# Performance work log

Measured on AMD Instinct MI355X. Metric: run time of the kernel, lower is better.

The kernel has to match this reference:

```python
import jax, jax.numpy as jnp
import numpy as np

EPS = 1e-5
HD = 16          # hidden_dim
OC = 256         # out_chs
NH = 8           # num_heads (groups of qkv conv)
DV = OC // (2 * HD)  # per-head value dim = 8


def conv_bn_silu(x, w, gamma, beta, mean, var, stride=1, pad=1, groups=1):
    # Conv2d(bias=False) + BatchNorm2d(eval) + SiLU, NCHW/OIHW
    y = jax.lax.conv_general_dilated(
        x, w, (stride, stride), [(pad, pad), (pad, pad)],
        dimension_numbers=('NCHW', 'OIHW', 'NCHW'),
        feature_group_count=groups)
    inv = gamma * jax.lax.rsqrt(var + EPS)
    y = y * inv[None, :, None, None] + (beta - mean * inv)[None, :, None, None]
    return y * jax.nn.sigmoid(y)


def _bn_params(key, c):
    k1, k2, k3, k4 = jax.random.split(key, 4)
    g = 1.0 + 0.1 * jax.random.normal(k1, (c,), jnp.float32)
    b = 0.1 * jax.random.normal(k2, (c,), jnp.float32)
    m = 0.1 * jax.random.normal(k3, (c,), jnp.float32)
    v = jax.random.uniform(k4, (c,), jnp.float32, 0.5, 1.5)
    return g, b, m, v


def setup_inputs() -> dict:
    key = jax.random.key(0)
    ks = jax.random.split(key, 8)
    B, C, H, W = 16, 256, 80, 80
    qkv_out = HD * 2 + OC // 2  # 160
    d = {}
    d['x'] = jax.random.normal(ks[0], (B, C, H, W), jnp.float32)
    # qkv_conv: grouped 3x3, groups=NH -> in per group = C//NH
    d['qkv_w'] = jax.random.normal(ks[1], (qkv_out, C // NH, 3, 3), jnp.float32) * 0.05
    d['qkv_g'], d['qkv_b'], d['qkv_m'], d['qkv_v'] = _bn_params(ks[2], qkv_out)
    # hidden_conv: dense 3x3
    d['hid_w'] = jax.random.normal(ks[3], (OC, C, 3, 3), jnp.float32) * 0.02
    d['hid_g'], d['hid_b'], d['hid_m'], d['hid_v'] = _bn_params(ks[4], OC)
    # out_conv: 1x1 on (OC//2*3) channels
    d['out_w'] = jax.random.normal(ks[5], (OC, OC // 2 * 3, 1, 1), jnp.float32) * 0.05
    d['out_g'], d['out_b'], d['out_m'], d['out_v'] = _bn_params(ks[6], OC)
    return d


def reference(x, qkv_w, qkv_g, qkv_b, qkv_m, qkv_v,
              hid_w, hid_g, hid_b, hid_m, hid_v,
              out_w, out_g, out_b, out_m, out_v):
    B, C, H, W = x.shape
    N = H * W
    qkv = conv_bn_silu(x, qkv_w, qkv_g, qkv_b, qkv_m, qkv_v, stride=1, pad=1, groups=NH)
    q = qkv[:, :HD]               # (B, HD, H, W)
    k = qkv[:, HD:2 * HD]
    v = qkv[:, 2 * HD:]           # (B, OC//2, H, W)
    # permute to (B, N, HD) / (B, N, HD, DV), channel-major reshape matches torch .view
    q = q.transpose(0, 2, 3, 1).reshape(B, N, HD)
    k = k.transpose(0, 2, 3, 1).reshape(B, N, HD)
    v = v.transpose(0, 2, 3, 1).reshape(B, N, HD, DV)
    # per-pixel tiny attention: attn[b,n,i,j] = softmax_j(q_i * k_j)
    attn = jax.nn.softmax(q[..., :, None] * k[..., None, :], axis=-1)  # (B,N,HD,HD)
    y = jnp.einsum('bnij,bnjd->bnid', attn, v)                          # (B,N,HD,DV)
    # torch: permute(0,2,3,1).view(B, OC//2, H, W)
    y = y.transpose(0, 2, 3, 1).reshape(B, OC // 2, H, W)
    h = conv_bn_silu(x, hid_w, hid_g, hid_b, hid_m, hid_v, stride=1, pad=1)
    y = jnp.concatenate([y, h], axis=1)  # (B, OC//2*3, H, W)
    return conv_bn_silu(y, out_w, out_g, out_b, out_m, out_v, stride=1, pad=0)
```

## Files before the change

kernel.cpp:

```cpp
#include <hip/hip_runtime.h>
#include <stdint.h>

typedef unsigned short u16;
typedef unsigned int u32;
typedef __attribute__((ext_vector_type(4))) float f32x4;
typedef __attribute__((ext_vector_type(8))) __bf16 bf16x8;

#define EPS_BN 1e-5f

__device__ __forceinline__ u16 f2bf(float f) {
  u32 u = __builtin_bit_cast(u32, f);
  u32 r = (u + 0x7fffu + ((u >> 16) & 1u)) >> 16;
  return (u16)r;
}

__device__ __forceinline__ float silu_f(float v) {
  return v / (1.0f + __expf(-v));
}

__device__ __forceinline__ void gll16(const void* g, void* l) {
  __builtin_amdgcn_global_load_lds(
      (__attribute__((address_space(1))) void*)(void*)g,
      (__attribute__((address_space(3))) void*)l, 16, 0, 0);
}

__global__ __launch_bounds__(256) void prep(
    const float* __restrict__ qkv_w, const float* __restrict__ qg,
    const float* __restrict__ qb, const float* __restrict__ qm,
    const float* __restrict__ qv,
    const float* __restrict__ hid_w, const float* __restrict__ hg,
    const float* __restrict__ hb, const float* __restrict__ hm,
    const float* __restrict__ hv,
    const float* __restrict__ out_w, const float* __restrict__ og,
    const float* __restrict__ ob, const float* __restrict__ om,
    const float* __restrict__ ov,
    u16* __restrict__ wtb, u16* __restrict__ w2b, u16* __restrict__ wqp,
    float* __restrict__ bnq_s, float* __restrict__ bnq_b,
    float* __restrict__ bnh_s, float* __restrict__ bnh_b,
    float* __restrict__ bn2s, float* __restrict__ bn2b,
    float* __restrict__ zpg)
{
  const int gid = blockIdx.x * 256 + threadIdx.x;
  if (gid < 256 * 2304) {
    int j = gid / 2304, k = gid - j * 2304;
    int tap = k >> 8, c = k & 255;
    wtb[gid] = f2bf(hid_w[(j * 256 + c) * 9 + tap]);
  }
  if (gid < 73728) {
    int g = gid / 9216;
    int r = gid - g * 9216;
    int j = r / 288, k = r - j * 288;
    int tap = k >> 5, cg = k & 31;
    float v = 0.f;
    if (j < 20) v = qkv_w[((g * 20 + j) * 32 + cg) * 9 + tap];
    wqp[gid] = f2bf(v);
  }
  if (gid < 98304) w2b[gid] = f2bf(out_w[gid]);
  if (gid < 160) {
    float iv = qg[gid] * rsqrtf(qv[gid] + EPS_BN);
    bnq_s[gid] = iv; bnq_b[gid] = qb[gid] - qm[gid] * iv;
  }
  if (gid < 256) {
    float iv = hg[gid] * rsqrtf(hv[gid] + EPS_BN);
    bnh_s[gid] = iv; bnh_b[gid] = hb[gid] - hm[gid] * iv;
    float iv2 = og[gid] * rsqrtf(ov[gid] + EPS_BN);
    bn2s[gid] = iv2; bn2b[gid] = ob[gid] - om[gid] * iv2;
  }
  if (gid < 64) zpg[gid] = 0.f;
}

__global__ __launch_bounds__(256) void nchw2nhwc(
    const float* __restrict__ x, u16* __restrict__ xn)
{
  __shared__ u16 T[80 * 66];
  const int t = threadIdx.x;
  const int ct = blockIdx.x;
  const int h  = blockIdx.y;
  const int b  = blockIdx.z;
  const float* src = x + ((size_t)b * 256 + ct * 64) * 6400 + h * 80;
  for (int it = 0; it < 20; ++it) {
    int idx = it * 256 + t;
    int cl = idx / 80, wl = idx - cl * 80;
    T[wl * 66 + cl] = f2bf(src[(size_t)cl * 6400 + wl]);
  }
  __syncthreads();
  u16* dst = xn + ((size_t)(b * 80 + h) * 80) * 256 + ct * 64;
  for (int it = 0; it < 5; ++it) {
    int idx = it * 256 + t;
    int wl = idx >> 4;
    int cl = (idx & 15) * 4;
    ushort4 v4;
    v4.x = T[wl * 66 + cl + 0];
    v4.y = T[wl * 66 + cl + 1];
    v4.z = T[wl * 66 + cl + 2];
    v4.w = T[wl * 66 + cl + 3];
    *(ushort4*)(dst + (size_t)wl * 256 + cl) = v4;
  }
}

__global__ __launch_bounds__(256, 2) void gemm_main(
    const u16* __restrict__ xn, const u16* __restrict__ wt,
    const float* __restrict__ bns, const float* __restrict__ bnb,
    const float* __restrict__ zpg, u16* __restrict__ ycat)
{
  __shared__ __attribute__((aligned(16))) u16 Al[128 * 64];
  __shared__ __attribute__((aligned(16))) u16 Bl[128 * 64];
  const int t = threadIdx.x;
  const int wave = t >> 6, lane = t & 63;
  const int wr = wave >> 1, wc = wave & 1;
  const int orig = blockIdx.y * 2 + blockIdx.x;
  const int wg = (orig & 7) * 200 + (orig >> 3);
  const int jtile = (wg / 800) * 128;
  const int ptile = (wg % 800) * 128;

  const int srcc = (((lane & 7) ^ ((lane >> 3) & 7)) * 8);
  int pb[4], hh[4], wwv[4], bofB[4];
#pragma unroll
  for (int c = 0; c < 4; ++c) {
    int m = wave * 32 + c * 8 + (lane >> 3);
    int p = ptile + m;
    pb[c] = p;
    int hw = p % 6400;
    hh[c] = hw / 80;
    wwv[c] = hw - (hw / 80) * 80;
    bofB[c] = (jtile + m) * 2304 + srcc;
  }
  u16* AlW = Al + wave * 2048;
  u16* BlW = Bl + wave * 2048;

  f32x4 acc[4][4];
#pragma unroll
  for (int m = 0; m < 4; ++m)
#pragma unroll
    for (int n = 0; n < 4; ++n) {
      f32x4 z = {0.f, 0.f, 0.f, 0.f};
      acc[m][n] = z;
    }

  for (int ks = 0; ks < 36; ++ks) {
    const int k0 = ks * 64;
    const int tap = k0 >> 8;
    const int c0 = k0 & 255;
    const int dh = tap / 3 - 1, dw = tap - (tap / 3) * 3 - 1;
    __syncthreads();
#pragma unroll
    for (int c = 0; c < 4; ++c) {
      int h2 = hh[c] + dh, w2 = wwv[c] + dw;
      bool ok = ((unsigned)h2 < 80u) & ((unsigned)w2 < 80u);
      const u16* src = ok
          ? (xn + ((size_t)(pb[c] + dh * 80 + dw) * 256 + c0 + srcc))
          : (const u16*)zpg;
      gll16(src, AlW + c * 512);
    }
#pragma unroll
    for (int c = 0; c < 4; ++c)
      gll16(wt + (size_t)(bofB[c] + k0), BlW + c * 512);
    __syncthreads();
#pragma unroll
    for (int kk = 0; kk < 2; ++kk) {
      const int q = kk * 4 + (lane >> 4);
      const int c16 = lane & 15;
      bf16x8 av[4], bv[4];
#pragma unroll
      for (int m = 0; m < 4; ++m) {
        int r = wr * 64 + m * 16 + c16;
        av[m] = *(const bf16x8*)(Al + r * 64 + (q ^ (r & 7)) * 8);
      }
#pragma unroll
      for (int n = 0; n < 4; ++n) {
        int r = wc * 64 + n * 16 + c16;
        bv[n] = *(const bf16x8*)(Bl + r * 64 + (q ^ (r & 7)) * 8);
      }
#pragma unroll
      for (int m = 0; m < 4; ++m)
#pragma unroll
        for (int n = 0; n < 4; ++n)
          acc[m][n] = __builtin_amdgcn_mfma_f32_16x16x32_bf16(
              av[m], bv[n], acc[m][n], 0, 0, 0);
    }
  }

  const int c16 = lane & 15, rg = lane >> 4;
#pragma unroll
  for (int n = 0; n < 4; ++n) {
    int j = jtile + wc * 64 + n * 16 + c16;
    float sc = bns[j], bi = bnb[j];
#pragma unroll
    for (int m = 0; m < 4; ++m) {
      int p0 = ptile + wr * 64 + m * 16 + rg * 4;
#pragma unroll
      for (int r = 0; r < 4; ++r) {
        float v = silu_f(acc[m][n][r] * sc + bi);
        ycat[(size_t)(p0 + r) * 384 + 128 + j] = f2bf(v);
      }
    }
  }
}

__global__ __launch_bounds__(256) void qkv_gemm(
    const u16* __restrict__ xn, const u16* __restrict__ wqp,
    const float* __restrict__ bnq_s, const float* __restrict__ bnq_b,
    float* __restrict__ qkvb)
{
  __shared__ __attribute__((aligned(16))) u16 Bs[32 * 296];
  const int t = threadIdx.x;
  const int wave = t >> 6, lane = t & 63;
  const int g = blockIdx.y;
  const int pt0 = blockIdx.x * 256;

  for (int idx = t; idx < 9216; idx += 256) {
    int j = idx / 288, k = idx - j * 288;
    Bs[j * 296 + k] = wqp[(size_t)(g * 32 + j) * 288 + k];
  }
  __syncthreads();

  const int c16 = lane & 15, q = lane >> 4;
  int pix[4], ph[4], pw[4];
#pragma unroll
  for (int m = 0; m < 4; ++m) {
    pix[m] = pt0 + wave * 64 + m * 16 + c16;
    int hw = pix[m] % 6400;
    ph[m] = hw / 80;
    pw[m] = hw - (hw / 80) * 80;
  }
  f32x4 acc[4][2];
#pragma unroll
  for (int m = 0; m < 4; ++m)
#pragma unroll
    for (int n = 0; n < 2; ++n) {
      f32x4 z = {0.f, 0.f, 0.f, 0.f};
      acc[m][n] = z;
    }
  bf16x8 zv;
#pragma unroll
  for (int i = 0; i < 8; ++i) zv[i] = (__bf16)0.0f;

#pragma unroll
  for (int tap = 0; tap < 9; ++tap) {
    const int dh = tap / 3 - 1, dw = tap - (tap / 3) * 3 - 1;
    const int dp = dh * 80 + dw;
    const bf16x8 bv0 = *(const bf16x8*)(Bs + c16 * 296 + tap * 32 + q * 8);
    const bf16x8 bv1 = *(const bf16x8*)(Bs + (16 + c16) * 296 + tap * 32 + q * 8);
#pragma unroll
    for (int m = 0; m < 4; ++m) {
      bool ok = ((unsigned)(ph[m] + dh) < 80u) & ((unsigned)(pw[m] + dw) < 80u);
      const bf16x8 raw = *(const bf16x8*)(
          xn + (long)(pix[m] + dp) * 256 + g * 32 + q * 8);
      const bf16x8 av = ok ? raw : zv;
      acc[m][0] = __builtin_amdgcn_mfma_f32_16x16x32_bf16(av, bv0, acc[m][0], 0, 0, 0);
      acc[m][1] = __builtin_amdgcn_mfma_f32_16x16x32_bf16(av, bv1, acc[m][1], 0, 0, 0);
    }
  }

#pragma unroll
  for (int n = 0; n < 2; ++n) {
    int jj = n * 16 + c16;
    if (jj < 20) {
      int oc = g * 20 + jj;
      float sc = bnq_s[oc], bi = bnq_b[oc];
#pragma unroll
      for (int m = 0; m < 4; ++m) {
        int p0 = pt0 + wave * 64 + m * 16 + q * 4;
#pragma unroll
        for (int r = 0; r < 4; ++r)
          qkvb[(size_t)(p0 + r) * 160 + oc] = silu_f(acc[m][n][r] * sc + bi);
      }
    }
  }
}

__global__ __launch_bounds__(256) void attn_k(
    const float* __restrict__ qkvb, u16* __restrict__ ycat)
{
  __shared__ float qs[16 * 168];
  const int t = threadIdx.x;
  const size_t p0 = (size_t)blockIdx.x * 16;
  const float* src = qkvb + p0 * 160;
  for (int idx = t; idx < 2560; idx += 256) {
    int r = idx / 160;
    qs[r * 168 + (idx - r * 160)] = src[idx];
  }
  __syncthreads();
  const int px = t >> 4, i = t & 15;
  const float* row = qs + px * 168;
  const float qi = row[i];
  float s[16];
  float mx = -3.4e38f;
#pragma unroll
  for (int j = 0; j < 16; ++j) { s[j] = qi * row[16 + j]; mx = fmaxf(mx, s[j]); }
  float sum = 0.f;
#pragma unroll
  for (int j = 0; j < 16; ++j) { s[j] = __expf(s[j] - mx); sum += s[j]; }
  const float inv = 1.0f / sum;
  float y[8];
#pragma unroll
  for (int d = 0; d < 8; ++d) y[d] = 0.f;
#pragma unroll
  for (int j = 0; j < 16; ++j) {
    const float a = s[j];
    const float* vr = row + 32 + j * 8;
#pragma unroll
    for (int d = 0; d < 8; ++d) y[d] += a * vr[d];
  }
  union { u16 u[8]; uint4 v4; } pk;
#pragma unroll
  for (int d = 0; d < 8; ++d) pk.u[d] = f2bf(y[d] * inv);
  *(uint4*)(ycat + (p0 + px) * 384 + i * 8) = pk.v4;
}

__global__ __launch_bounds__(256, 2) void gemm_out(
    const u16* __restrict__ w2, const u16* __restrict__ ycat,
    const float* __restrict__ bns, const float* __restrict__ bnb,
    float* __restrict__ out)
{
  __shared__ __attribute__((aligned(16))) u16 Al[128 * 64];
  __shared__ __attribute__((aligned(16))) u16 Bl[128 * 64];
  const int t = threadIdx.x;
  const int wave = t >> 6, lane = t & 63;
  const int wr = wave >> 1, wc = wave & 1;
  const int orig = blockIdx.y * 2 + blockIdx.x;
  const int wg = (orig & 7) * 200 + (orig >> 3);
  const int octile = (wg / 800) * 128;
  const int ptile = (wg % 800) * 128;

  const int srcc = (((lane & 7) ^ ((lane >> 3) & 7)) * 8);
  int bofA[4], bofB[4];
#pragma unroll
  for (int c = 0; c < 4; ++c) {
    int m = wave * 32 + c * 8 + (lane >> 3);
    bofA[c] = (octile + m) * 384 + srcc;
    bofB[c] = (ptile + m) * 384 + srcc;
  }
  u16* AlW = Al + wave * 2048;
  u16* BlW = Bl + wave * 2048;

  f32x4 acc[4][4];
#pragma unroll
  for (int m = 0; m < 4; ++m)
#pragma unroll
    for (int n = 0; n < 4; ++n) {
      f32x4 z = {0.f, 0.f, 0.f, 0.f};
      acc[m][n] = z;
    }

  for (int ks = 0; ks < 6; ++ks) {
    const int k0 = ks * 64;
    __syncthreads();
#pragma unroll
    for (int c = 0; c < 4; ++c) gll16(w2 + (size_t)(bofA[c] + k0), AlW + c * 512);
#pragma unroll
    for (int c = 0; c < 4; ++c) gll16(ycat + (size_t)(bofB[c] + k0), BlW + c * 512);
    __syncthreads();
#pragma unroll
    for (int kk = 0; kk < 2; ++kk) {
      const int q = kk * 4 + (lane >> 4);
      const int c16 = lane & 15;
      bf16x8 av[4], bv[4];
#pragma unroll
      for (int m = 0; m < 4; ++m) {
        int r = wr * 64 + m * 16 + c16;
        av[m] = *(const bf16x8*)(Al + r * 64 + (q ^ (r & 7)) * 8);
      }
#pragma unroll
      for (int n = 0; n < 4; ++n) {
        int r = wc * 64 + n * 16 + c16;
        bv[n] = *(const bf16x8*)(Bl + r * 64 + (q ^ (r & 7)) * 8);
      }
#pragma unroll
      for (int m = 0; m < 4; ++m)
#pragma unroll
        for (int n = 0; n < 4; ++n)
          acc[m][n] = __builtin_amdgcn_mfma_f32_16x16x32_bf16(
              av[m], bv[n], acc[m][n], 0, 0, 0);
    }
  }

  const int c16 = lane & 15, rg = lane >> 4;
  const int b = ptile / 6400;
  const int hwb = ptile - b * 6400;
#pragma unroll
  for (int m = 0; m < 4; ++m) {
    int oc0 = octile + wr * 64 + m * 16 + rg * 4;
#pragma unroll
    for (int n = 0; n < 4; ++n) {
      int hw = hwb + wc * 64 + n * 16 + c16;
#pragma unroll
      for (int r = 0; r < 4; ++r) {
        int oc = oc0 + r;
        float v = silu_f(acc[m][n][r] * bns[oc] + bnb[oc]);
        out[((size_t)b * 256 + oc) * 6400 + hw] = v;
      }
    }
  }
}

extern "C" void kernel_launch(void* const* d_in, const int* in_sizes, int n_in,
                              void* d_out, int out_size, void* d_ws, size_t ws_size,
                              hipStream_t stream) {
  (void)in_sizes; (void)n_in; (void)out_size; (void)ws_size;
  const float* x    = (const float*)d_in[0];
  const float* qkvw = (const float*)d_in[1];
  const float* qg   = (const float*)d_in[2];
  const float* qb   = (const float*)d_in[3];
  const float* qm   = (const float*)d_in[4];
  const float* qv   = (const float*)d_in[5];
  const float* hw_  = (const float*)d_in[6];
  const float* hg   = (const float*)d_in[7];
  const float* hb   = (const float*)d_in[8];
  const float* hm   = (const float*)d_in[9];
  const float* hv   = (const float*)d_in[10];
  const float* ow   = (const float*)d_in[11];
  const float* og   = (const float*)d_in[12];
  const float* ob   = (const float*)d_in[13];
  const float* om   = (const float*)d_in[14];
  const float* ov   = (const float*)d_in[15];

  char* ws = (char*)d_ws;
  float* zpg   = (float*)(ws + 0);
  float* bnq_s = (float*)(ws + 256);
  float* bnq_b = (float*)(ws + 1280);
  float* bnh_s = (float*)(ws + 2304);
  float* bnh_b = (float*)(ws + 3328);
  float* bn2s  = (float*)(ws + 4352);
  float* bn2b  = (float*)(ws + 5376);
  u16*   wtb   = (u16*)(ws + 6400);
  u16*   w2b   = (u16*)(ws + 1186048);
  u16*   wqp   = (u16*)(ws + 1382656);
  u16*   xn    = (u16*)(ws + 1536000);
  float* qkvb  = (float*)(ws + 53964800);
  u16*   ycat  = (u16*)(ws + 119500800);
  float* out   = (float*)d_out;

  prep<<<dim3(2304), dim3(256), 0, stream>>>(
      qkvw, qg, qb, qm, qv, hw_, hg, hb, hm, hv, ow, og, ob, om, ov,
      wtb, w2b, wqp, bnq_s, bnq_b, bnh_s, bnh_b, bn2s, bn2b, zpg);
  nchw2nhwc<<<dim3(4, 80, 16), dim3(256), 0, stream>>>(x, xn);
  gemm_main<<<dim3(2, 800), dim3(256), 0, stream>>>(
      xn, wtb, bnh_s, bnh_b, zpg, ycat);
  qkv_gemm<<<dim3(400, 8), dim3(256), 0, stream>>>(
      xn, wqp, bnq_s, bnq_b, qkvb);
  attn_k<<<dim3(6400), dim3(256), 0, stream>>>(qkvb, ycat);
  gemm_out<<<dim3(2, 800), dim3(256), 0, stream>>>(
      w2b, ycat, bn2s, bn2b, out);
}
```

Measured before the change: 356.0 us.

## Restructure grouped qkv conv to stage all-group pixel tiles via LDS async loads

The grouped 3x3 qkv convolution now runs one block per 128-pixel tile across all 8 groups. Each 64-channel input slice is staged into swizzled LDS with global_load_lds and padding is redirected to a zero buffer. This replaces the old per-group grid, where each block re-read strided 16-byte chunks straight from global memory. Separately, the NCHW-to-NHWC transpose now reads float4 vectors instead of scalars. The new qkv kernel holds 32 accumulator fragments per thread, which raises register pressure, and it loads weights from global memory on every k-step.

```diff
diff --git a/kernel.cpp b/kernel.cpp
--- a/kernel.cpp
+++ b/kernel.cpp
@@ -78,10 +78,14 @@
   const int h  = blockIdx.y;
   const int b  = blockIdx.z;
   const float* src = x + ((size_t)b * 256 + ct * 64) * 6400 + h * 80;
-  for (int it = 0; it < 20; ++it) {
+  for (int it = 0; it < 5; ++it) {
     int idx = it * 256 + t;
-    int cl = idx / 80, wl = idx - cl * 80;
-    T[wl * 66 + cl] = f2bf(src[(size_t)cl * 6400 + wl]);
+    int cl = idx / 20, w4 = idx - cl * 20;
+    float4 v = *(const float4*)(src + (size_t)cl * 6400 + w4 * 4);
+    T[(w4 * 4 + 0) * 66 + cl] = f2bf(v.x);
+    T[(w4 * 4 + 1) * 66 + cl] = f2bf(v.y);
+    T[(w4 * 4 + 2) * 66 + cl] = f2bf(v.z);
+    T[(w4 * 4 + 3) * 66 + cl] = f2bf(v.w);
   }
   __syncthreads();
   u16* dst = xn + ((size_t)(b * 80 + h) * 80) * 256 + ct * 64;
@@ -197,74 +201,98 @@
   }
 }
 
-__global__ __launch_bounds__(256) void qkv_gemm(
+__global__ __launch_bounds__(256, 2) void qkv_gemm(
     const u16* __restrict__ xn, const u16* __restrict__ wqp,
     const float* __restrict__ bnq_s, const float* __restrict__ bnq_b,
-    float* __restrict__ qkvb)
-{
-  __shared__ __attribute__((aligned(16))) u16 Bs[32 * 296];
+    const float* __restrict__ zpg, float* __restrict__ qkvb)
+{
+  __shared__ __attribute__((aligned(16))) u16 Al[128 * 64];
   const int t = threadIdx.x;
   const int wave = t >> 6, lane = t & 63;
-  const int g = blockIdx.y;
-  const int pt0 = blockIdx.x * 256;
-
-  for (int idx = t; idx < 9216; idx += 256) {
-    int j = idx / 288, k = idx - j * 288;
-    Bs[j * 296 + k] = wqp[(size_t)(g * 32 + j) * 288 + k];
-  }
-  __syncthreads();
-
-  const int c16 = lane & 15, q = lane >> 4;
-  int pix[4], ph[4], pw[4];
-#pragma unroll
-  for (int m = 0; m < 4; ++m) {
-    pix[m] = pt0 + wave * 64 + m * 16 + c16;
-    int hw = pix[m] % 6400;
-    ph[m] = hw / 80;
-    pw[m] = hw - (hw / 80) * 80;
-  }
-  f32x4 acc[4][2];
-#pragma unroll
-  for (int m = 0; m < 4; ++m)
-#pragma unroll
-    for (int n = 0; n < 2; ++n) {
+  const int orig = blockIdx.x;
+  const int wg = (orig & 7) * 100 + (orig >> 3);
+  const int ptile = wg * 128;
+
+  const int srcc = (((lane & 7) ^ ((lane >> 3) & 7)) * 8);
+  int pb[4], hh[4], wwv[4];
+#pragma unroll
+  for (int c = 0; c < 4; ++c) {
+    int m = wave * 32 + c * 8 + (lane >> 3);
+    int p = ptile + m;
+    pb[c] = p;
+    int hw = p % 6400;
+    hh[c] = hw / 80;
+    wwv[c] = hw - (hw / 80) * 80;
+  }
+  u16* AlW = Al + wave * 2048;
+
+  const int q = lane >> 4, c16 = lane & 15;
+  f32x4 acc[2][16];
+#pragma unroll
+  for (int m = 0; m < 2; ++m)
+#pragma unroll
+    for (int f = 0; f < 16; ++f) {
       f32x4 z = {0.f, 0.f, 0.f, 0.f};
-      acc[m][n] = z;
-    }
-  bf16x8 zv;
-#pragma unroll
-  for (int i = 0; i < 8; ++i) zv[i] = (__bf16)0.0f;
-
-#pragma unroll
-  for (int tap = 0; tap < 9; ++tap) {
+      acc[m][f] = z;
+    }
+
+  for (int ks = 0; ks < 36; ++ks) {
+    const int k0 = ks * 64;
+    const int tap = k0 >> 8;
+    const int c0 = k0 & 255;
+    const int cc = ks & 3;
     const int dh = tap / 3 - 1, dw = tap - (tap / 3) * 3 - 1;
-    const int dp = dh * 80 + dw;
-    const bf16x8 bv0 = *(const bf16x8*)(Bs + c16 * 296 + tap * 32 + q * 8);
-    const bf16x8 bv1 = *(const bf16x8*)(Bs + (16 + c16) * 296 + tap * 32 + q * 8);
-#pragma unroll
-    for (int m = 0; m < 4; ++m) {
-      bool ok = ((unsigned)(ph[m] + dh) < 80u) & ((unsigned)(pw[m] + dw) < 80u);
-      const bf16x8 raw = *(const bf16x8*)(
-          xn + (long)(pix[m] + dp) * 256 + g * 32 + q * 8);
-      const bf16x8 av = ok ? raw : zv;
-      acc[m][0] = __builtin_amdgcn_mfma_f32_16x16x32_bf16(av, bv0, acc[m][0], 0, 0, 0);
-      acc[m][1] = __builtin_amdgcn_mfma_f32_16x16x32_bf16(av, bv1, acc[m][1], 0, 0, 0);
-    }
-  }
-
-#pragma unroll
-  for (int n = 0; n < 2; ++n) {
-    int jj = n * 16 + c16;
-    if (jj < 20) {
-      int oc = g * 20 + jj;
-      float sc = bnq_s[oc], bi = bnq_b[oc];
-#pragma unroll
-      for (int m = 0; m < 4; ++m) {
-        int p0 = pt0 + wave * 64 + m * 16 + q * 4;
-#pragma unroll
-        for (int r = 0; r < 4; ++r)
-          qkvb[(size_t)(p0 + r) * 160 + oc] = silu_f(acc[m][n][r] * sc + bi);
-      }
+    __syncthreads();
+#pragma unroll
+    for (int c = 0; c < 4; ++c) {
+      int h2 = hh[c] + dh, w2 = wwv[c] + dw;
+      bool ok = ((unsigned)h2 < 80u) & ((unsigned)w2 < 80u);
+      const u16* src = ok
+          ? (xn + ((size_t)(pb[c] + dh * 80 + dw) * 256 + c0 + srcc))
+          : (const u16*)zpg;
+      gll16(src, AlW + c * 512);
+    }
+    bf16x8 bv[2][2];
+#pragma unroll
+    for (int h = 0; h < 2; ++h)
+#pragma unroll
+      for (int nf = 0; nf < 2; ++nf) {
+        int row = (2 * cc + h) * 32 + nf * 16 + c16;
+        bv[h][nf] = *(const bf16x8*)(wqp + (size_t)row * 288 + tap * 32 + q * 8);
+      }
+    __syncthreads();
+    bf16x8 av[2][2];
+#pragma unroll
+    for (int m = 0; m < 2; ++m) {
+      int r = wave * 32 + m * 16 + c16;
+#pragma unroll
+      for (int h = 0; h < 2; ++h) {
+        int q8 = h * 4 + q;
+        av[m][h] = *(const bf16x8*)(Al + r * 64 + (q8 ^ (r & 7)) * 8);
+      }
+    }
+#pragma unroll
+    for (int h = 0; h < 2; ++h)
+#pragma unroll
+      for (int m = 0; m < 2; ++m)
+#pragma unroll
+        for (int nf = 0; nf < 2; ++nf)
+          acc[m][(2 * cc + h) * 2 + nf] = __builtin_amdgcn_mfma_f32_16x16x32_bf16(
+              av[m][h], bv[h][nf], acc[m][(2 * cc + h) * 2 + nf], 0, 0, 0);
+  }
+
+#pragma unroll
+  for (int f = 0; f < 16; ++f) {
+    int jj = (f & 1) * 16 + c16;
+    if (jj >= 20) continue;
+    int oc = (f >> 1) * 20 + jj;
+    float sc = bnq_s[oc], bi = bnq_b[oc];
+#pragma unroll
+    for (int m = 0; m < 2; ++m) {
+      int p0 = ptile + wave * 32 + m * 16 + q * 4;
+#pragma unroll
+      for (int r = 0; r < 4; ++r)
+        qkvb[(size_t)(p0 + r) * 160 + oc] = silu_f(acc[m][f][r] * sc + bi);
     }
   }
 }
@@ -437,8 +465,8 @@
   nchw2nhwc<<<dim3(4, 80, 16), dim3(256), 0, stream>>>(x, xn);
   gemm_main<<<dim3(2, 800), dim3(256), 0, stream>>>(
       xn, wtb, bnh_s, bnh_b, zpg, ycat);
-  qkv_gemm<<<dim3(400, 8), dim3(256), 0, stream>>>(
-      xn, wqp, bnq_s, bnq_b, qkvb);
+  qkv_gemm<<<dim3(800), dim3(256), 0, stream>>>(
+      xn, wqp, bnq_s, bnq_b, zpg, qkvb);
   attn_k<<<dim3(6400), dim3(256), 0, stream>>>(qkvb, ycat);
   gemm_out<<<dim3(2, 800), dim3(256), 0, stream>>>(
       w2b, ycat, bn2s, bn2b, out);
```

After: 749.7 us. 2.11x slower.

## Fuse grouped qkv conv into main hidden-conv GEMM and vectorize NCHW transpose loads

Applied to the files above, without the earlier changes.

Drops the separate qkv_gemm kernel. The grouped 3x3 qkv convolution is now computed inside gemm_main, reusing the activation tiles already staged in LDS. Each output-column tile handles the qkv groups whose 32 input channels fall in its k-slice, and the weights come straight from global memory. This removes a second full read of xn and one kernel launch, at the cost of 64 extra accumulator registers per thread, which may hurt occupancy under launch_bounds(256,2). The NCHW-to-NHWC transpose also switches to float4 global loads.

```diff
diff --git a/kernel.cpp b/kernel.cpp
--- a/kernel.cpp
+++ b/kernel.cpp
@@ -78,10 +78,14 @@
   const int h  = blockIdx.y;
   const int b  = blockIdx.z;
   const float* src = x + ((size_t)b * 256 + ct * 64) * 6400 + h * 80;
-  for (int it = 0; it < 20; ++it) {
+  for (int it = 0; it < 5; ++it) {
     int idx = it * 256 + t;
-    int cl = idx / 80, wl = idx - cl * 80;
-    T[wl * 66 + cl] = f2bf(src[(size_t)cl * 6400 + wl]);
+    int cl = idx / 20, w4 = idx - cl * 20;
+    float4 v = *(const float4*)(src + (size_t)cl * 6400 + w4 * 4);
+    T[(w4 * 4 + 0) * 66 + cl] = f2bf(v.x);
+    T[(w4 * 4 + 1) * 66 + cl] = f2bf(v.y);
+    T[(w4 * 4 + 2) * 66 + cl] = f2bf(v.z);
+    T[(w4 * 4 + 3) * 66 + cl] = f2bf(v.w);
   }
   __syncthreads();
   u16* dst = xn + ((size_t)(b * 80 + h) * 80) * 256 + ct * 64;
@@ -100,8 +104,11 @@
 
 __global__ __launch_bounds__(256, 2) void gemm_main(
     const u16* __restrict__ xn, const u16* __restrict__ wt,
+    const u16* __restrict__ wqp,
     const float* __restrict__ bns, const float* __restrict__ bnb,
-    const float* __restrict__ zpg, u16* __restrict__ ycat)
+    const float* __restrict__ bnq_s, const float* __restrict__ bnq_b,
+    const float* __restrict__ zpg, u16* __restrict__ ycat,
+    float* __restrict__ qkvb)
 {
   __shared__ __attribute__((aligned(16))) u16 Al[128 * 64];
   __shared__ __attribute__((aligned(16))) u16 Bl[128 * 64];
@@ -110,7 +117,8 @@
   const int wr = wave >> 1, wc = wave & 1;
   const int orig = blockIdx.y * 2 + blockIdx.x;
   const int wg = (orig & 7) * 200 + (orig >> 3);
-  const int jtile = (wg / 800) * 128;
+  const int jt = wg / 800;
+  const int jtile = jt * 128;
   const int ptile = (wg % 800) * 128;
 
   const int srcc = (((lane & 7) ^ ((lane >> 3) & 7)) * 8);
@@ -128,6 +136,8 @@
   u16* AlW = Al + wave * 2048;
   u16* BlW = Bl + wave * 2048;
 
+  const int c16 = lane & 15, lq = lane >> 4;
+
   f32x4 acc[4][4];
 #pragma unroll
   for (int m = 0; m < 4; ++m)
@@ -136,51 +146,81 @@
       f32x4 z = {0.f, 0.f, 0.f, 0.f};
       acc[m][n] = z;
     }
-
-  for (int ks = 0; ks < 36; ++ks) {
-    const int k0 = ks * 64;
-    const int tap = k0 >> 8;
-    const int c0 = k0 & 255;
+  f32x4 acc_q[2][8];
+#pragma unroll
+  for (int m = 0; m < 2; ++m)
+#pragma unroll
+    for (int f = 0; f < 8; ++f) {
+      f32x4 z = {0.f, 0.f, 0.f, 0.f};
+      acc_q[m][f] = z;
+    }
+
+  for (int tap = 0; tap < 9; ++tap) {
     const int dh = tap / 3 - 1, dw = tap - (tap / 3) * 3 - 1;
-    __syncthreads();
+    const int dp = dh * 80 + dw;
+    const u16* srcA[4];
 #pragma unroll
     for (int c = 0; c < 4; ++c) {
       int h2 = hh[c] + dh, w2 = wwv[c] + dw;
       bool ok = ((unsigned)h2 < 80u) & ((unsigned)w2 < 80u);
-      const u16* src = ok
-          ? (xn + ((size_t)(pb[c] + dh * 80 + dw) * 256 + c0 + srcc))
-          : (const u16*)zpg;
-      gll16(src, AlW + c * 512);
-    }
-#pragma unroll
-    for (int c = 0; c < 4; ++c)
-      gll16(wt + (size_t)(bofB[c] + k0), BlW + c * 512);
-    __syncthreads();
-#pragma unroll
-    for (int kk = 0; kk < 2; ++kk) {
-      const int q = kk * 4 + (lane >> 4);
-      const int c16 = lane & 15;
-      bf16x8 av[4], bv[4];
-#pragma unroll
-      for (int m = 0; m < 4; ++m) {
-        int r = wr * 64 + m * 16 + c16;
-        av[m] = *(const bf16x8*)(Al + r * 64 + (q ^ (r & 7)) * 8);
-      }
-#pragma unroll
-      for (int n = 0; n < 4; ++n) {
-        int r = wc * 64 + n * 16 + c16;
-        bv[n] = *(const bf16x8*)(Bl + r * 64 + (q ^ (r & 7)) * 8);
-      }
-#pragma unroll
-      for (int m = 0; m < 4; ++m)
-#pragma unroll
-        for (int n = 0; n < 4; ++n)
-          acc[m][n] = __builtin_amdgcn_mfma_f32_16x16x32_bf16(
-              av[m], bv[n], acc[m][n], 0, 0, 0);
-    }
-  }
-
-  const int c16 = lane & 15, rg = lane >> 4;
+      srcA[c] = ok ? (xn + ((size_t)(pb[c] + dp) * 256 + srcc))
+                   : (const u16*)zpg;
+    }
+#pragma unroll
+    for (int cc = 0; cc < 4; ++cc) {
+      const int c0 = cc * 64;
+      const int k0 = tap * 256 + c0;
+      __syncthreads();
+#pragma unroll
+      for (int c = 0; c < 4; ++c)
+        gll16(srcA[c] == (const u16*)zpg ? srcA[c] : srcA[c] + c0,
+              AlW + c * 512);
+#pragma unroll
+      for (int c = 0; c < 4; ++c)
+        gll16(wt + (size_t)(bofB[c] + k0), BlW + c * 512);
+      const int gq = 2 * cc + jt;
+      const bf16x8 bq0 = *(const bf16x8*)(
+          wqp + ((size_t)(gq * 32) + c16) * 288 + tap * 32 + lq * 8);
+      const bf16x8 bq1 = *(const bf16x8*)(
+          wqp + ((size_t)(gq * 32) + 16 + c16) * 288 + tap * 32 + lq * 8);
+      __syncthreads();
+#pragma unroll
+      for (int kk = 0; kk < 2; ++kk) {
+        const int q = kk * 4 + lq;
+        bf16x8 av[4], bv[4];
+#pragma unroll
+        for (int m = 0; m < 4; ++m) {
+          int r = wr * 64 + m * 16 + c16;
+          av[m] = *(const bf16x8*)(Al + r * 64 + (q ^ (r & 7)) * 8);
+        }
+#pragma unroll
+        for (int n = 0; n < 4; ++n) {
+          int r = wc * 64 + n * 16 + c16;
+          bv[n] = *(const bf16x8*)(Bl + r * 64 + (q ^ (r & 7)) * 8);
+        }
+#pragma unroll
+        for (int m = 0; m < 4; ++m)
+#pragma unroll
+          for (int n = 0; n < 4; ++n)
+            acc[m][n] = __builtin_amdgcn_mfma_f32_16x16x32_bf16(
+                av[m], bv[n], acc[m][n], 0, 0, 0);
+        if (kk == jt) {
+          const bf16x8 aq0 = wc ? av[2] : av[0];
+          const bf16x8 aq1 = wc ? av[3] : av[1];
+          acc_q[0][cc * 2 + 0] = __builtin_amdgcn_mfma_f32_16x16x32_bf16(
+              aq0, bq0, acc_q[0][cc * 2 + 0], 0, 0, 0);
+          acc_q[0][cc * 2 + 1] = __builtin_amdgcn_mfma_f32_16x16x32_bf16(
+              aq0, bq1, acc_q[0][cc * 2 + 1], 0, 0, 0);
+          acc_q[1][cc * 2 + 0] = __builtin_amdgcn_mfma_f32_16x16x32_bf16(
+              aq1, bq0, acc_q[1][cc * 2 + 0], 0, 0, 0);
+          acc_q[1][cc * 2 + 1] = __builtin_amdgcn_mfma_f32_16x16x32_bf16(
+              aq1, bq1, acc_q[1][cc * 2 + 1], 0, 0, 0);
+        }
+      }
+    }
+  }
+
+  const int rg = lq;
 #pragma unroll
   for (int n = 0; n < 4; ++n) {
     int j = jtile + wc * 64 + n * 16 + c16;
@@ -195,75 +235,23 @@
       }
     }
   }
-}
-
-__global__ __launch_bounds__(256) void qkv_gemm(
-    const u16* __restrict__ xn, const u16* __restrict__ wqp,
-    const float* __restrict__ bnq_s, const float* __restrict__ bnq_b,
-    float* __restrict__ qkvb)
-{
-  __shared__ __attribute__((aligned(16))) u16 Bs[32 * 296];
-  const int t = threadIdx.x;
-  const int wave = t >> 6, lane = t & 63;
-  const int g = blockIdx.y;
-  const int pt0 = blockIdx.x * 256;
-
-  for (int idx = t; idx < 9216; idx += 256) {
-    int j = idx / 288, k = idx - j * 288;
-    Bs[j * 296 + k] = wqp[(size_t)(g * 32 + j) * 288 + k];
-  }
-  __syncthreads();
-
-  const int c16 = lane & 15, q = lane >> 4;
-  int pix[4], ph[4], pw[4];
-#pragma unroll
-  for (int m = 0; m < 4; ++m) {
-    pix[m] = pt0 + wave * 64 + m * 16 + c16;
-    int hw = pix[m] % 6400;
-    ph[m] = hw / 80;
-    pw[m] = hw - (hw / 80) * 80;
-  }
-  f32x4 acc[4][2];
-#pragma unroll
-  for (int m = 0; m < 4; ++m)
-#pragma unroll
-    for (int n = 0; n < 2; ++n) {
-      f32x4 z = {0.f, 0.f, 0.f, 0.f};
-      acc[m][n] = z;
-    }
-  bf16x8 zv;
-#pragma unroll
-  for (int i = 0; i < 8; ++i) zv[i] = (__bf16)0.0f;
-
-#pragma unroll
-  for (int tap = 0; tap < 9; ++tap) {
-    const int dh = tap / 3 - 1, dw = tap - (tap / 3) * 3 - 1;
-    const int dp = dh * 80 + dw;
-    const bf16x8 bv0 = *(const bf16x8*)(Bs + c16 * 296 + tap * 32 + q * 8);
-    const bf16x8 bv1 = *(const bf16x8*)(Bs + (16 + c16) * 296 + tap * 32 + q * 8);
-#pragma unroll
-    for (int m = 0; m < 4; ++m) {
-      bool ok = ((unsigned)(ph[m] + dh) < 80u) & ((unsigned)(pw[m] + dw) < 80u);
-      const bf16x8 raw = *(const bf16x8*)(
-          xn + (long)(pix[m] + dp) * 256 + g * 32 + q * 8);
-      const bf16x8 av = ok ? raw : zv;
-      acc[m][0] = __builtin_amdgcn_mfma_f32_16x16x32_bf16(av, bv0, acc[m][0], 0, 0, 0);
-      acc[m][1] = __builtin_amdgcn_mfma_f32_16x16x32_bf16(av, bv1, acc[m][1], 0, 0, 0);
-    }
-  }
-
-#pragma unroll
-  for (int n = 0; n < 2; ++n) {
-    int jj = n * 16 + c16;
-    if (jj < 20) {
-      int oc = g * 20 + jj;
-      float sc = bnq_s[oc], bi = bnq_b[oc];
-#pragma unroll
-      for (int m = 0; m < 4; ++m) {
-        int p0 = pt0 + wave * 64 + m * 16 + q * 4;
-#pragma unroll
-        for (int r = 0; r < 4; ++r)
-          qkvb[(size_t)(p0 + r) * 160 + oc] = silu_f(acc[m][n][r] * sc + bi);
+#pragma unroll
+  for (int cc = 0; cc < 4; ++cc) {
+    int gq = 2 * cc + jt;
+#pragma unroll
+    for (int nf = 0; nf < 2; ++nf) {
+      int jj = nf * 16 + c16;
+      if (jj < 20) {
+        int oc = gq * 20 + jj;
+        float sc = bnq_s[oc], bi = bnq_b[oc];
+#pragma unroll
+        for (int m2 = 0; m2 < 2; ++m2) {
+          int p0 = ptile + wr * 64 + wc * 32 + m2 * 16 + rg * 4;
+#pragma unroll
+          for (int r = 0; r < 4; ++r)
+            qkvb[(size_t)(p0 + r) * 160 + oc] =
+                silu_f(acc_q[m2][cc * 2 + nf][r] * sc + bi);
+        }
       }
     }
   }
@@ -436,9 +424,7 @@
       wtb, w2b, wqp, bnq_s, bnq_b, bnh_s, bnh_b, bn2s, bn2b, zpg);
   nchw2nhwc<<<dim3(4, 80, 16), dim3(256), 0, stream>>>(x, xn);
   gemm_main<<<dim3(2, 800), dim3(256), 0, stream>>>(
-      xn, wtb, bnh_s, bnh_b, zpg, ycat);
-  qkv_gemm<<<dim3(400, 8), dim3(256), 0, stream>>>(
-      xn, wqp, bnq_s, bnq_b, qkvb);
+      xn, wtb, wqp, bnh_s, bnh_b, bnq_s, bnq_b, zpg, ycat, qkvb);
   attn_k<<<dim3(6400), dim3(256), 0, stream>>>(qkvb, ycat);
   gemm_out<<<dim3(2, 800), dim3(256), 0, stream>>>(
       w2b, ycat, bn2s, bn2b, out);
```

Result: slower. 385.5 us (+8.3%).
